# Performance work log

Hardware: AMD Instinct MI355X
Metric: run time of the kernel (lower is better)

Reference implementation:

```python
import jax, jax.numpy as jnp
import numpy as np

N_NODES = 100000
N_EDGES = 1600000
F_IN = 128
HID = 128  # nhid*2
NHID = 64
N_GRAPHS = 512
N_CLASSES = 10
NEG_SLOPE = 0.2  # PyG GATConv default


def setup_inputs() -> dict:
    key = jax.random.key(0)
    ks = jax.random.split(key, 16)
    x = jax.random.normal(ks[0], (N_NODES, F_IN), dtype=jnp.float32)
    edge_index = jax.random.randint(ks[1], (2, N_EDGES), 0, N_NODES, dtype=jnp.int64)
    batch = jnp.sort(jax.random.randint(ks[2], (N_NODES,), 0, N_GRAPHS, dtype=jnp.int64))
    def lin(k, fan_in, shape):
        bound = 1.0 / np.sqrt(fan_in)
        return jax.random.uniform(k, shape, jnp.float32, -bound, bound)
    return {
        "x": x, "edge_index": edge_index, "batch": batch,
        "W1": lin(ks[3], F_IN, (F_IN, HID)),
        "a_src1": lin(ks[4], HID, (HID,)),
        "a_dst1": lin(ks[5], HID, (HID,)),
        "b1": jnp.zeros((HID,), jnp.float32),
        "W2": lin(ks[6], HID, (HID, HID)),
        "a_src2": lin(ks[7], HID, (HID,)),
        "a_dst2": lin(ks[8], HID, (HID,)),
        "b2": jnp.zeros((HID,), jnp.float32),
        "W_fc1": lin(ks[9], HID, (HID, NHID)),
        "b_fc1": lin(ks[10], HID, (NHID,)),
        "W_fc2": lin(ks[11], NHID, (NHID, N_CLASSES)),
        "b_fc2": lin(ks[12], NHID, (N_CLASSES,)),
    }


def gat_conv(x, src, dst, W, a_src, a_dst, b):
    # h = W x ; attention e_ij = LeakyReLU(a_src.h_i + a_dst.h_j), softmax over
    # incoming edges of each destination j, then scatter-add aggregation.
    h = x @ W                                   # [N, H]
    alpha_s = h @ a_src                         # [N]
    alpha_d = h @ a_dst                         # [N]
    e = jax.nn.leaky_relu(alpha_s[src] + alpha_d[dst], NEG_SLOPE)  # [E]
    n = x.shape[0]
    m = jax.ops.segment_max(e, dst, num_segments=n)                # per-dst max
    ex = jnp.exp(e - m[dst])
    denom = jax.ops.segment_sum(ex, dst, num_segments=n)
    alpha = ex / denom[dst]                                        # [E]
    out = jax.ops.segment_sum(alpha[:, None] * h[src], dst, num_segments=n)
    return out + b


def reference(x, edge_index, batch, W1, a_src1, a_dst1, b1,
              W2, a_src2, a_dst2, b2, W_fc1, b_fc1, W_fc2, b_fc2):
    n = x.shape[0]
    # GATConv default add_self_loops=True
    loops = jnp.arange(n, dtype=edge_index.dtype)
    src = jnp.concatenate([edge_index[0], loops])
    dst = jnp.concatenate([edge_index[1], loops])

    h = jax.nn.selu(gat_conv(x, src, dst, W1, a_src1, a_dst1, b1))
    h = jax.nn.selu(gat_conv(h, src, dst, W2, a_src2, a_dst2, b2))

    # global mean pool over graphs
    sums = jax.ops.segment_sum(h, batch, num_segments=N_GRAPHS)
    cnts = jax.ops.segment_sum(jnp.ones((n,), h.dtype), batch, num_segments=N_GRAPHS)
    pooled = jax.nn.selu(sums / jnp.maximum(cnts, 1.0)[:, None])   # [G, H]

    g = jax.nn.selu(pooled @ W_fc1 + b_fc1)
    # dropout p=0.5 is identity in eval mode
    logits = g @ W_fc2 + b_fc2
    return jax.nn.log_softmax(logits, axis=-1)
```

## Files before the change

kernel.cpp:

```cpp
#include <hip/hip_runtime.h>
#include <hip/hip_bf16.h>

#define NEG_SLOPE 0.2f
typedef unsigned int uint32;

#define BSHIFT 9
#define BSIZE 512
#define MAXB 256
#define PCHUNK 2048
#define PEPT 8
#define BSTRIDE 12288
#define PNODES 256
#define PSPAN 16

typedef __attribute__((ext_vector_type(8))) __bf16 bf16x8;
typedef __attribute__((ext_vector_type(4))) float f32x4;
typedef __attribute__((ext_vector_type(2))) float f32x2;

__device__ __forceinline__ float selu_f(float x) {
    const float a = 1.6732632423543772f, s = 1.0507009873554805f;
    return x > 0.0f ? s * x : s * a * (__expf(x) - 1.0f);
}

__device__ __forceinline__ unsigned short f2bf(float x) {
    uint32 u = __float_as_uint(x);
    uint32 r = (u + 0x7fff + ((u >> 16) & 1)) >> 16;
    return (unsigned short)r;
}
__device__ __forceinline__ float bf_lo(uint32 g) { return __uint_as_float(g << 16); }
__device__ __forceinline__ float bf_hi(uint32 g) { return __uint_as_float(g & 0xffff0000u); }

__device__ __forceinline__ f32x2 f8x2lo(uint32 w) { return __builtin_amdgcn_cvt_pk_f32_fp8((int)w, false); }
__device__ __forceinline__ f32x2 f8x2hi(uint32 w) { return __builtin_amdgcn_cvt_pk_f32_fp8((int)w, true); }

__global__ __launch_bounds__(256) void prep9(const float* __restrict__ W1,
                                             const float* __restrict__ W2,
                                             unsigned short* __restrict__ Wb,
                                             const int* __restrict__ batch,
                                             int* __restrict__ gstart,
                                             int* __restrict__ gcur0,
                                             float* __restrict__ gsum,
                                             int N, int G) {
    int b = blockIdx.x, t = threadIdx.x;
    if (b < 2) {
        if (b == 0 && t < MAXB) gcur0[t] = 0;
        const float* W = b ? W2 : W1;
        unsigned short* oh = Wb + (size_t)b * 32768;
        unsigned short* ol = oh + 16384;
        for (int d = t; d < 16384; d += 256) {
            int j = d & 7, nn = (d >> 3) & 127, g = d >> 10;
            float v = W[(g * 8 + j) * 128 + nn];
            uint32 hu = f2bf(v);
            float hv = __uint_as_float(hu << 16);
            oh[d] = (unsigned short)hu;
            ol[d] = f2bf(v - hv);
        }
    } else {
        int i = (b - 2) * 256 + t;
        if (i < G * 128) gsum[i] = 0.0f;
        if (i < N) {
            int bb = batch[i];
            int bp = (i == 0) ? -1 : batch[i - 1];
            for (int q = bp + 1; q <= bb; ++q) gstart[q] = i;
            if (i == N - 1)
                for (int q = bb + 1; q <= G; ++q) gstart[q] = N;
        }
    }
}

__global__ __launch_bounds__(256) void partition_edges(const int* __restrict__ ei,
                                                       int* __restrict__ gcur0,
                                                       uint32* __restrict__ tmp,
                                                       int E, int TOT) {
    __shared__ int lcnt[MAXB];
    __shared__ int lstart[MAXB];
    __shared__ int lcur[MAXB];
    __shared__ int gbase[MAXB];
    __shared__ int wsums[4];
    __shared__ uint32 staged[PCHUNK];
    __shared__ unsigned char bslot[PCHUNK];
    int t = threadIdx.x;
    int lane = t & 63, w = t >> 6;
    int eb = blockIdx.x * PCHUNK;
    int sreg[PEPT], dreg[PEPT];
    #pragma unroll
    for (int k = 0; k < PEPT; ++k) {
        int e = eb + k * 256 + t;
        if (e < TOT) {
            if (e < E) { sreg[k] = ei[e]; dreg[k] = ei[E + e]; }
            else       { sreg[k] = dreg[k] = e - E; }
        } else dreg[k] = -1;
    }
    lcnt[t] = 0;
    __syncthreads();
    #pragma unroll
    for (int k = 0; k < PEPT; ++k)
        if (dreg[k] >= 0) atomicAdd(&lcnt[dreg[k] >> BSHIFT], 1);
    __syncthreads();
    int v = lcnt[t];
    int incl = v;
    #pragma unroll
    for (int off = 1; off < 64; off <<= 1) {
        int u = __shfl_up(incl, off);
        if (lane >= off) incl += u;
    }
    if (lane == 63) wsums[w] = incl;
    __syncthreads();
    int wadd = 0;
    #pragma unroll
    for (int k = 0; k < 4; ++k) wadd += (k < w) ? wsums[k] : 0;
    int ex = incl + wadd - v;
    lstart[t] = ex;
    lcur[t] = ex;
    if (v > 0) gbase[t] = t * BSTRIDE + atomicAdd(&gcur0[t], v);
    __syncthreads();
    #pragma unroll
    for (int k = 0; k < PEPT; ++k) {
        int d = dreg[k];
        if (d >= 0) {
            int b = d >> BSHIFT;
            int p = atomicAdd(&lcur[b], 1);
            staged[p] = ((uint32)(d & (BSIZE - 1)) << 17) | (uint32)sreg[k];
            bslot[p] = (unsigned char)b;
        }
    }
    __syncthreads();
    int nvalid = TOT - eb; if (nvalid > PCHUNK) nvalid = PCHUNK;
    for (int i = t; i < nvalid; i += 256) {
        int b = bslot[i];
        tmp[gbase[b] + (i - lstart[b])] = staged[i];
    }
}

__global__ __launch_bounds__(1024) void bucket_build(const uint32* __restrict__ tmp,
                                                     const int* __restrict__ gcur0,
                                                     int* __restrict__ rowptr,
                                                     int* __restrict__ rowend,
                                                     int* __restrict__ col,
                                                     int N, int NB) {
    __shared__ int cnt[BSIZE];
    __shared__ int bsums[4];
    int b = blockIdx.x, t = threadIdx.x;
    int lo = b << BSHIFT;
    int nn = N - lo; if (nn > BSIZE) nn = BSIZE;
    if (t < BSIZE) cnt[t] = 0;
    __syncthreads();
    int ebeg = b * BSTRIDE;
    int eend = ebeg + gcur0[b];
    for (int i = ebeg + t; i < eend; i += 1024)
        atomicAdd(&cnt[tmp[i] >> 17], 1);
    __syncthreads();
    int c0 = 0, c1 = 0, s2 = 0;
    if (t < 256) {
        c0 = cnt[2 * t]; c1 = cnt[2 * t + 1];
        s2 = c0 + c1;
    }
    int lane = t & 63, w = t >> 6;
    int incl = s2;
    #pragma unroll
    for (int off = 1; off < 64; off <<= 1) {
        int u = __shfl_up(incl, off);
        if (lane >= off) incl += u;
    }
    if (t < 256 && lane == 63) bsums[w] = incl;
    __syncthreads();
    if (t < 256) {
        int wadd = 0;
        #pragma unroll
        for (int k = 0; k < 4; ++k) wadd += (k < w) ? bsums[k] : 0;
        int ex = incl + wadd - s2;
        int st0 = ebeg + ex, st1 = st0 + c0;
        if (2 * t < nn)     { rowptr[lo + 2 * t] = st0;     rowend[lo + 2 * t] = st0 + c0; }
        if (2 * t + 1 < nn) { rowptr[lo + 2 * t + 1] = st1; rowend[lo + 2 * t + 1] = st1 + c1; }
        cnt[2 * t] = st0; cnt[2 * t + 1] = st1;
    }
    __syncthreads();
    for (int i = ebeg + t; i < eend; i += 1024) {
        uint32 u = tmp[i];
        int p = atomicAdd(&cnt[u >> 17], 1);
        col[p] = (int)(u & 0x1FFFFu);
    }
}

template<bool FP8>
__device__ __forceinline__ void gemm_core(const bf16x8 ah[2][4],
                                          const __bf16* Wl,
                                          const float* a_src, const float* a_dst,
                                          uint32* hb, float* as_, float* ad_,
                                          int rbase, int n, int col16, int quad) {
    f32x4 acc[2][8];
    #pragma unroll
    for (int mt = 0; mt < 2; ++mt)
        #pragma unroll
        for (int t = 0; t < 8; ++t) acc[mt][t] = (f32x4)(0.0f);

    #pragma unroll
    for (int c = 0; c < 4; ++c) {
        #pragma unroll
        for (int t = 0; t < 8; ++t) {
            int off = (((c * 4 + quad) * 128) + t * 16 + col16) * 8;
            bf16x8 bh = *(const bf16x8*)&Wl[off];
            bf16x8 bl = *(const bf16x8*)&Wl[16384 + off];
            #pragma unroll
            for (int mt = 0; mt < 2; ++mt) {
                acc[mt][t] = __builtin_amdgcn_mfma_f32_16x16x32_bf16(ah[mt][c], bh, acc[mt][t], 0, 0, 0);
                acc[mt][t] = __builtin_amdgcn_mfma_f32_16x16x32_bf16(ah[mt][c], bl, acc[mt][t], 0, 0, 0);
            }
        }
    }
    float asv[8], adv[8];
    #pragma unroll
    for (int t = 0; t < 8; ++t) { asv[t] = a_src[t * 16 + col16]; adv[t] = a_dst[t * 16 + col16]; }
    #pragma unroll
    for (int mt = 0; mt < 2; ++mt) {
        #pragma unroll
        for (int reg = 0; reg < 4; ++reg) {
            float s = 0.0f, d = 0.0f;
            #pragma unroll
            for (int t = 0; t < 8; ++t) {
                float v = acc[mt][t][reg];
                s += v * asv[t]; d += v * adv[t];
            }
            #pragma unroll
            for (int off = 1; off < 16; off <<= 1) {
                s += __shfl_xor(s, off);
                d += __shfl_xor(d, off);
            }
            int r = rbase + mt * 16 + quad * 4 + reg;
            if (col16 == 0 && r < n) { as_[r] = s; ad_[r] = d; }
        }
    }
    #pragma unroll
    for (int mt = 0; mt < 2; ++mt)
    #pragma unroll
    for (int t = 0; t < 8; ++t)
    #pragma unroll
    for (int reg = 0; reg < 4; ++reg) {
        float v = acc[mt][t][reg];
        int r = rbase + mt * 16 + quad * 4 + reg;
        if (FP8) {
            float p1 = __shfl_xor(v, 1);
            uint32 pk = (uint32)__builtin_amdgcn_cvt_pk_fp8_f32(v, p1, 0, false);
            uint32 pk2 = __shfl_xor(pk, 2);
            if (!(col16 & 3) && r < n)
                hb[(size_t)r * 32 + t * 4 + (col16 >> 2)] = (pk & 0xffffu) | (pk2 << 16);
        } else {
            float p = __shfl_xor(v, 1);
            if (!(col16 & 1) && r < n) {
                uint32 pkb = (uint32)f2bf(v) | ((uint32)f2bf(p) << 16);
                hb[(size_t)r * 64 + t * 8 + (col16 >> 1)] = pkb;
            }
        }
    }
}

__global__ __launch_bounds__(512) void gemm_mfma_f32(const float* __restrict__ X,
                                                     const unsigned short* __restrict__ Wbh,
                                                     const float* __restrict__ a_src,
                                                     const float* __restrict__ a_dst,
                                                     uint32* __restrict__ hb,
                                                     float* __restrict__ as_,
                                                     float* __restrict__ ad_, int n) {
    __shared__ __bf16 Wl[32768];
    const int tid = threadIdx.x;
    {
        const uint4* sw = (const uint4*)Wbh;
        uint4* dw = (uint4*)Wl;
        for (int i = tid; i < 4096; i += 512) dw[i] = sw[i];
    }
    const int lane = tid & 63, wid = tid >> 6;
    const int col16 = lane & 15, quad = lane >> 4;
    const int rbase = blockIdx.x * 256 + wid * 32;
    bf16x8 ah[2][4];
    #pragma unroll
    for (int mt = 0; mt < 2; ++mt) {
        int r = rbase + mt * 16 + col16;
        bool ok = (r < n);
        const float* xp = X + (size_t)r * 128;
        #pragma unroll
        for (int c = 0; c < 4; ++c) {
            int k0 = c * 32 + quad * 8;
            float4 x0 = ok ? *(const float4*)(xp + k0)     : make_float4(0.f,0.f,0.f,0.f);
            float4 x1 = ok ? *(const float4*)(xp + k0 + 4) : make_float4(0.f,0.f,0.f,0.f);
            float xs[8] = {x0.x,x0.y,x0.z,x0.w,x1.x,x1.y,x1.z,x1.w};
            #pragma unroll
            for (int j = 0; j < 8; ++j) ah[mt][c][j] = (__bf16)xs[j];
        }
    }
    __syncthreads();
    gemm_core<true>(ah, Wl, a_src, a_dst, hb, as_, ad_, rbase, n, col16, quad);
}

__global__ __launch_bounds__(512) void gemm_mfma_bf16(const __bf16* __restrict__ X,
                                                      const unsigned short* __restrict__ Wbh,
                                                      const float* __restrict__ a_src,
                                                      const float* __restrict__ a_dst,
                                                      uint32* __restrict__ hb,
                                                      float* __restrict__ as_,
                                                      float* __restrict__ ad_, int n) {
    __shared__ __bf16 Wl[32768];
    const int tid = threadIdx.x;
    {
        const uint4* sw = (const uint4*)Wbh;
        uint4* dw = (uint4*)Wl;
        for (int i = tid; i < 4096; i += 512) dw[i] = sw[i];
    }
    const int lane = tid & 63, wid = tid >> 6;
    const int col16 = lane & 15, quad = lane >> 4;
    const int rbase = blockIdx.x * 256 + wid * 32;
    bf16x8 ah[2][4];
    const bf16x8 zz = (bf16x8)((__bf16)0.0f);
    #pragma unroll
    for (int mt = 0; mt < 2; ++mt) {
        int r = rbase + mt * 16 + col16;
        bool ok = (r < n);
        const __bf16* xp = X + (size_t)r * 128;
        #pragma unroll
        for (int c = 0; c < 4; ++c)
            ah[mt][c] = ok ? *(const bf16x8*)(xp + c * 32 + quad * 8) : zz;
    }
    __syncthreads();
    gemm_core<true>(ah, Wl, a_src, a_dst, hb, as_, ad_, rbase, n, col16, quad);
}

#define GIDX8(SARR, T0) { _Pragma("unroll") \
    for (int k_ = 0; k_ < 8; ++k_) { int t_ = (T0) + k_; \
        int sv_ = (t_ < 16) ? s0 : s1; \
        int si_ = __shfl(sv_, base + (t_ & 15)); \
        SARR[k_] = (t_ < cnt) ? si_ : 0; } }

#define GW8(WARR, T0) { _Pragma("unroll") \
    for (int k_ = 0; k_ < 8; ++k_) { int t_ = (T0) + k_; \
        float wv_ = (t_ < 16) ? w0 : w1; \
        float wf_ = __shfl(wv_, base + (t_ & 15)); \
        WARR[k_] = (t_ < cnt) ? wf_ : 0.0f; } }

#define GLOAD8_F8(GARR, SARR) { _Pragma("unroll") \
    for (int k_ = 0; k_ < 8; ++k_) GARR[k_] = hb2[(uint32)SARR[k_] * 16u + l]; }

#define GCONSUME_F8(GARR, WARR) { _Pragma("unroll") \
    for (int k_ = 0; k_ < 8; ++k_) { \
        f32x2 wv_ = (f32x2)WARR[k_]; \
        ac[0] = __builtin_elementwise_fma(wv_, f8x2lo(GARR[k_].x), ac[0]); \
        ac[1] = __builtin_elementwise_fma(wv_, f8x2hi(GARR[k_].x), ac[1]); \
        ac[2] = __builtin_elementwise_fma(wv_, f8x2lo(GARR[k_].y), ac[2]); \
        ac[3] = __builtin_elementwise_fma(wv_, f8x2hi(GARR[k_].y), ac[3]); } }

__global__ __launch_bounds__(256) void gat_csr5_f8(const int* __restrict__ rowptr,
                                                   const int* __restrict__ rowend,
                                                   const int* __restrict__ col,
                                                   const uint2* __restrict__ hb2,
                                                   const float* __restrict__ as_,
                                                   const float* __restrict__ ad_,
                                                   const float* __restrict__ bias,
                                                   uint4* __restrict__ outb, int n) {
    const int wid = threadIdx.x >> 6;
    const int lane = threadIdx.x & 63;
    const int q = lane >> 4, l = lane & 15;
    const int base = lane & 48;
    const int node = blockIdx.x * 16 + wid * 4 + q;
    const bool valid = node < n;
    int beg = 0, end = 0;
    if (valid) { beg = rowptr[node]; end = rowend[node]; }
    float add = valid ? ad_[node] : 0.0f;
    int deg = end - beg;
    int m1 = max(deg, __shfl_xor(deg, 16));
    int mdeg = max(m1, __shfl_xor(m1, 32));
    float s = 0.0f;
    f32x2 ac[4];
    #pragma unroll
    for (int p = 0; p < 4; ++p) ac[p] = (f32x2)(0.0f);

    for (int cb = 0; cb < mdeg; cb += 32) {
        int j0 = beg + cb + l, j1 = j0 + 16;
        bool e0 = (j0 < end), e1 = (j1 < end);
        int s0 = e0 ? col[j0] : 0;
        int s1 = e1 ? col[j1] : 0;
        int cnt = end - beg - cb;
        cnt = (cnt < 0) ? 0 : (cnt > 32 ? 32 : cnt);
        int rem = mdeg - cb; if (rem > 32) rem = 32;
        const int NB8 = (rem + 7) >> 3;

        int si[8]; uint2 gA[8], gB[8]; float wA[8], wB[8];

        GIDX8(si, 0); GLOAD8_F8(gA, si);

        float v0 = as_[s0] + add;
        float v1 = as_[s1] + add;
        v0 = (v0 > 0.0f) ? v0 : NEG_SLOPE * v0;
        v1 = (v1 > 0.0f) ? v1 : NEG_SLOPE * v1;
        float w0 = e0 ? __expf(v0) : 0.0f;
        float w1 = e1 ? __expf(v1) : 0.0f;
        float ws = w0 + w1;
        #pragma unroll
        for (int off = 8; off > 0; off >>= 1) ws += __shfl_xor(ws, off);
        s += ws;
        GW8(wA, 0);

        int b = 0;
        while (true) {
            bool moreB = (b + 1 < NB8);
            if (moreB) { GIDX8(si, (b + 1) * 8); GLOAD8_F8(gB, si); GW8(wB, (b + 1) * 8); }
            GCONSUME_F8(gA, wA);
            if (!moreB) break;
            bool moreA = (b + 2 < NB8);
            if (moreA) { GIDX8(si, (b + 2) * 8); GLOAD8_F8(gA, si); GW8(wA, (b + 2) * 8); }
            GCONSUME_F8(gB, wB);
            if (!moreA) break;
            b += 2;
        }
    }
    if (valid) {
        float inv = 1.0f / s;
        float4 b0 = *(const float4*)&bias[l * 8];
        float4 b1 = *(const float4*)&bias[l * 8 + 4];
        float r0 = selu_f(ac[0].x * inv + b0.x);
        float r1 = selu_f(ac[0].y * inv + b0.y);
        float r2 = selu_f(ac[1].x * inv + b0.z);
        float r3 = selu_f(ac[1].y * inv + b0.w);
        float r4 = selu_f(ac[2].x * inv + b1.x);
        float r5 = selu_f(ac[2].y * inv + b1.y);
        float r6 = selu_f(ac[3].x * inv + b1.z);
        float r7 = selu_f(ac[3].y * inv + b1.w);
        uint4 o;
        o.x = (uint32)f2bf(r0) | ((uint32)f2bf(r1) << 16);
        o.y = (uint32)f2bf(r2) | ((uint32)f2bf(r3) << 16);
        o.z = (uint32)f2bf(r4) | ((uint32)f2bf(r5) << 16);
        o.w = (uint32)f2bf(r6) | ((uint32)f2bf(r7) << 16);
        outb[(uint32)node * 16u + l] = o;
    }
}

__global__ __launch_bounds__(256) void pool_stream(const uint32* __restrict__ act,
                                                   const int* __restrict__ batch,
                                                   float* __restrict__ gsum, int N) {
    __shared__ float pacc[PSPAN][128];
    const int t = threadIdx.x, wid = t >> 6, u = t & 63;
    const int n0 = blockIdx.x * PNODES;
    int n1 = n0 + PNODES; if (n1 > N) n1 = N;
    for (int i = t; i < PSPAN * 128; i += 256) pacc[i >> 7][i & 127] = 0.f;
    __syncthreads();
    const int gfirst = batch[n0];
    float a0 = 0.f, a1 = 0.f;
    int gcur = gfirst;
    for (int nd = n0 + wid; nd < n1; nd += 4) {
        int g = batch[nd];
        if (g != gcur) {
            int slot = gcur - gfirst;
            if (slot < PSPAN) {
                atomicAdd(&pacc[slot][2 * u], a0);
                atomicAdd(&pacc[slot][2 * u + 1], a1);
            } else {
                atomicAdd(&gsum[(size_t)gcur * 128 + 2 * u], a0);
                atomicAdd(&gsum[(size_t)gcur * 128 + 2 * u + 1], a1);
            }
            a0 = a1 = 0.f; gcur = g;
        }
        uint32 gv = act[(size_t)nd * 64 + u];
        a0 += bf_lo(gv); a1 += bf_hi(gv);
    }
    {
        int slot = gcur - gfirst;
        if (slot < PSPAN) {
            atomicAdd(&pacc[slot][2 * u], a0);
            atomicAdd(&pacc[slot][2 * u + 1], a1);
        } else {
            atomicAdd(&gsum[(size_t)gcur * 128 + 2 * u], a0);
            atomicAdd(&gsum[(size_t)gcur * 128 + 2 * u + 1], a1);
        }
    }
    __syncthreads();
    int lastg = batch[n1 - 1];
    int nslots = lastg - gfirst + 1; if (nslots > PSPAN) nslots = PSPAN;
    for (int i = t; i < nslots * 128; i += 256) {
        float v = pacc[i >> 7][i & 127];
        if (v != 0.f)
            atomicAdd(&gsum[(size_t)(gfirst + (i >> 7)) * 128 + (i & 127)], v);
    }
}

__global__ __launch_bounds__(128) void pool_head2(const float* __restrict__ gsum,
                                                  const int* __restrict__ gstart,
                                                  const float* __restrict__ Wfc1,
                                                  const float* __restrict__ bfc1,
                                                  const float* __restrict__ Wfc2,
                                                  const float* __restrict__ bfc2,
                                                  float* __restrict__ out) {
    __shared__ float p[128];
    __shared__ float q[64];
    __shared__ float l[10];
    __shared__ float red[2];
    int g = blockIdx.x, t = threadIdx.x;
    int lo = gstart[g], hi = gstart[g + 1];
    float c = fmaxf((float)(hi - lo), 1.0f);
    p[t] = selu_f(gsum[(size_t)g * 128 + t] / c);
    __syncthreads();
    if (t < 64) {
        float a = bfc1[t];
        #pragma unroll 8
        for (int k = 0; k < 128; ++k) a += p[k] * Wfc1[k * 64 + t];
        q[t] = selu_f(a);
    }
    __syncthreads();
    if (t < 10) {
        float a = bfc2[t];
        #pragma unroll
        for (int k = 0; k < 64; ++k) a += q[k] * Wfc2[k * 10 + t];
        l[t] = a;
    }
    __syncthreads();
    if (t == 0) {
        float mx = l[0];
        for (int c2 = 1; c2 < 10; ++c2) mx = fmaxf(mx, l[c2]);
        float sum = 0.0f;
        for (int c2 = 0; c2 < 10; ++c2) sum += __expf(l[c2] - mx);
        red[0] = mx; red[1] = logf(sum);
    }
    __syncthreads();
    if (t < 10) out[g * 10 + t] = l[t] - red[0] - red[1];
}

extern "C" void kernel_launch(void* const* d_in, const int* in_sizes, int n_in,
                              void* d_out, int out_size, void* d_ws, size_t ws_size,
                              hipStream_t stream) {
    const float* x      = (const float*)d_in[0];
    const int*   ei     = (const int*)d_in[1];
    const int*   batch  = (const int*)d_in[2];
    const float* W1     = (const float*)d_in[3];
    const float* asrc1  = (const float*)d_in[4];
    const float* adst1  = (const float*)d_in[5];
    const float* b1     = (const float*)d_in[6];
    const float* W2     = (const float*)d_in[7];
    const float* asrc2  = (const float*)d_in[8];
    const float* adst2  = (const float*)d_in[9];
    const float* b2     = (const float*)d_in[10];
    const float* Wfc1   = (const float*)d_in[11];
    const float* bfc1   = (const float*)d_in[12];
    const float* Wfc2   = (const float*)d_in[13];
    const float* bfc2   = (const float*)d_in[14];
    float* out = (float*)d_out;

    const int N = in_sizes[0] / 128;
    const int E = in_sizes[1] / 2;
    const int G = out_size / 10;
    const int TOT = E + N;
    const int NB = ((N - 1) >> BSHIFT) + 1;
    const int GB = (N + 255) / 256;
    const int PH = (TOT + PCHUNK - 1) / PCHUNK;
    const int GemmG = (N + 255) / 256;

    uint32* hb    = (uint32*)d_ws;
    uint32* h2b   = hb + (size_t)N * 64;
    uint32* tmp   = h2b + (size_t)N * 64;
    int*    col   = (int*)(tmp + (size_t)NB * BSTRIDE);
    float* as_    = (float*)(col + (size_t)NB * BSTRIDE);
    float* ad_    = as_ + N;
    int*   gstart = (int*)(ad_ + N);
    int*   rowptr = gstart + (G + 2);
    int*   rowend = rowptr + (N + 2);
    int*   gcur0  = rowend + (N + 2);
    unsigned short* Wb = (unsigned short*)(((uintptr_t)(gcur0 + MAXB) + 255) & ~(uintptr_t)255);
    float* gsum = (float*)(Wb + 2 * 32768);

    const int gatGrid = (N + 15) / 16;

    prep9<<<2 + GB, 256, 0, stream>>>(W1, W2, Wb, batch, gstart, gcur0, gsum, N, G);
    partition_edges<<<PH, 256, 0, stream>>>(ei, gcur0, tmp, E, TOT);
    bucket_build<<<NB, 1024, 0, stream>>>(tmp, gcur0, rowptr, rowend, col, N, NB);

    gemm_mfma_f32<<<GemmG, 512, 0, stream>>>(x, Wb, asrc1, adst1, hb, as_, ad_, N);
    gat_csr5_f8<<<gatGrid, 256, 0, stream>>>(rowptr, rowend, col, (const uint2*)hb,
                                             as_, ad_, b1, (uint4*)h2b, N);

    gemm_mfma_bf16<<<GemmG, 512, 0, stream>>>((const __bf16*)h2b, Wb + 32768, asrc2, adst2, hb, as_, ad_, N);
    gat_csr5_f8<<<gatGrid, 256, 0, stream>>>(rowptr, rowend, col, (const uint2*)hb,
                                             as_, ad_, b2, (uint4*)h2b, N);

    pool_stream<<<(N + PNODES - 1) / PNODES, 256, 0, stream>>>(h2b, batch, gsum, N);
    pool_head2<<<G, 128, 0, stream>>>(gsum, gstart, Wfc1, bfc1, Wfc2, bfc2, out);
}
```

Before: 353.3 us.

## Split GAT edge gather into two half-waves with 16-byte row loads

Each 16-lane node group now splits into two 8-lane halves, and each half handles alternate edges. A lane loads a uint4 (16 fp8 features) per edge instead of a uint2, so each half-group gathers a full 128-byte row with wider loads. Partial accumulators from the two halves are combined with a cross-lane shuffle before the epilogue, and only half the lanes write the output. This halves the per-lane gather instruction count and raises bytes per load, at the cost of more accumulator registers and an extra reduction step.

```diff
diff --git a/kernel.cpp b/kernel.cpp
--- a/kernel.cpp
+++ b/kernel.cpp
@@ -323,33 +323,37 @@
     gemm_core<true>(ah, Wl, a_src, a_dst, hb, as_, ad_, rbase, n, col16, quad);
 }
 
-#define GIDX8(SARR, T0) { _Pragma("unroll") \
-    for (int k_ = 0; k_ < 8; ++k_) { int t_ = (T0) + k_; \
+#define GIDX4(SARR, T0) { _Pragma("unroll") \
+    for (int k_ = 0; k_ < 4; ++k_) { int t_ = (T0) + 2 * k_ + sub; \
         int sv_ = (t_ < 16) ? s0 : s1; \
         int si_ = __shfl(sv_, base + (t_ & 15)); \
         SARR[k_] = (t_ < cnt) ? si_ : 0; } }
 
-#define GW8(WARR, T0) { _Pragma("unroll") \
-    for (int k_ = 0; k_ < 8; ++k_) { int t_ = (T0) + k_; \
+#define GW4(WARR, T0) { _Pragma("unroll") \
+    for (int k_ = 0; k_ < 4; ++k_) { int t_ = (T0) + 2 * k_ + sub; \
         float wv_ = (t_ < 16) ? w0 : w1; \
         float wf_ = __shfl(wv_, base + (t_ & 15)); \
         WARR[k_] = (t_ < cnt) ? wf_ : 0.0f; } }
 
-#define GLOAD8_F8(GARR, SARR) { _Pragma("unroll") \
-    for (int k_ = 0; k_ < 8; ++k_) GARR[k_] = hb2[(uint32)SARR[k_] * 16u + l]; }
-
-#define GCONSUME_F8(GARR, WARR) { _Pragma("unroll") \
-    for (int k_ = 0; k_ < 8; ++k_) { \
+#define GLOAD4_F8(GARR, SARR) { _Pragma("unroll") \
+    for (int k_ = 0; k_ < 4; ++k_) GARR[k_] = hb4[(uint32)SARR[k_] * 8u + l7]; }
+
+#define GCONSUME4_F8(GARR, WARR) { _Pragma("unroll") \
+    for (int k_ = 0; k_ < 4; ++k_) { \
         f32x2 wv_ = (f32x2)WARR[k_]; \
         ac[0] = __builtin_elementwise_fma(wv_, f8x2lo(GARR[k_].x), ac[0]); \
         ac[1] = __builtin_elementwise_fma(wv_, f8x2hi(GARR[k_].x), ac[1]); \
         ac[2] = __builtin_elementwise_fma(wv_, f8x2lo(GARR[k_].y), ac[2]); \
-        ac[3] = __builtin_elementwise_fma(wv_, f8x2hi(GARR[k_].y), ac[3]); } }
-
-__global__ __launch_bounds__(256) void gat_csr5_f8(const int* __restrict__ rowptr,
+        ac[3] = __builtin_elementwise_fma(wv_, f8x2hi(GARR[k_].y), ac[3]); \
+        ac[4] = __builtin_elementwise_fma(wv_, f8x2lo(GARR[k_].z), ac[4]); \
+        ac[5] = __builtin_elementwise_fma(wv_, f8x2hi(GARR[k_].z), ac[5]); \
+        ac[6] = __builtin_elementwise_fma(wv_, f8x2lo(GARR[k_].w), ac[6]); \
+        ac[7] = __builtin_elementwise_fma(wv_, f8x2hi(GARR[k_].w), ac[7]); } }
+
+__global__ __launch_bounds__(256) void gat_csr6_f8(const int* __restrict__ rowptr,
                                                    const int* __restrict__ rowend,
                                                    const int* __restrict__ col,
-                                                   const uint2* __restrict__ hb2,
+                                                   const uint4* __restrict__ hb4,
                                                    const float* __restrict__ as_,
                                                    const float* __restrict__ ad_,
                                                    const float* __restrict__ bias,
@@ -358,6 +362,8 @@
     const int lane = threadIdx.x & 63;
     const int q = lane >> 4, l = lane & 15;
     const int base = lane & 48;
+    const int sub = (lane >> 3) & 1;
+    const int l7 = lane & 7;
     const int node = blockIdx.x * 16 + wid * 4 + q;
     const bool valid = node < n;
     int beg = 0, end = 0;
@@ -367,9 +373,9 @@
     int m1 = max(deg, __shfl_xor(deg, 16));
     int mdeg = max(m1, __shfl_xor(m1, 32));
     float s = 0.0f;
-    f32x2 ac[4];
-    #pragma unroll
-    for (int p = 0; p < 4; ++p) ac[p] = (f32x2)(0.0f);
+    f32x2 ac[8];
+    #pragma unroll
+    for (int p = 0; p < 8; ++p) ac[p] = (f32x2)(0.0f);
 
     for (int cb = 0; cb < mdeg; cb += 32) {
         int j0 = beg + cb + l, j1 = j0 + 16;
@@ -381,9 +387,9 @@
         int rem = mdeg - cb; if (rem > 32) rem = 32;
         const int NB8 = (rem + 7) >> 3;
 
-        int si[8]; uint2 gA[8], gB[8]; float wA[8], wB[8];
-
-        GIDX8(si, 0); GLOAD8_F8(gA, si);
+        int si[4]; uint4 gA[4], gB[4]; float wA[4], wB[4];
+
+        GIDX4(si, 0); GLOAD4_F8(gA, si);
 
         float v0 = as_[s0] + add;
         float v1 = as_[s1] + add;
@@ -395,39 +401,40 @@
         #pragma unroll
         for (int off = 8; off > 0; off >>= 1) ws += __shfl_xor(ws, off);
         s += ws;
-        GW8(wA, 0);
+        GW4(wA, 0);
 
         int b = 0;
         while (true) {
             bool moreB = (b + 1 < NB8);
-            if (moreB) { GIDX8(si, (b + 1) * 8); GLOAD8_F8(gB, si); GW8(wB, (b + 1) * 8); }
-            GCONSUME_F8(gA, wA);
+            if (moreB) { GIDX4(si, (b + 1) * 8); GLOAD4_F8(gB, si); GW4(wB, (b + 1) * 8); }
+            GCONSUME4_F8(gA, wA);
             if (!moreB) break;
             bool moreA = (b + 2 < NB8);
-            if (moreA) { GIDX8(si, (b + 2) * 8); GLOAD8_F8(gA, si); GW8(wA, (b + 2) * 8); }
-            GCONSUME_F8(gB, wB);
+            if (moreA) { GIDX4(si, (b + 2) * 8); GLOAD4_F8(gA, si); GW4(wA, (b + 2) * 8); }
+            GCONSUME4_F8(gB, wB);
             if (!moreA) break;
             b += 2;
         }
     }
-    if (valid) {
+    float e[16];
+    #pragma unroll
+    for (int i = 0; i < 8; ++i) {
+        e[2 * i]     = ac[i].x + __shfl_xor(ac[i].x, 8);
+        e[2 * i + 1] = ac[i].y + __shfl_xor(ac[i].y, 8);
+    }
+    if (valid && sub == 0) {
         float inv = 1.0f / s;
-        float4 b0 = *(const float4*)&bias[l * 8];
-        float4 b1 = *(const float4*)&bias[l * 8 + 4];
-        float r0 = selu_f(ac[0].x * inv + b0.x);
-        float r1 = selu_f(ac[0].y * inv + b0.y);
-        float r2 = selu_f(ac[1].x * inv + b0.z);
-        float r3 = selu_f(ac[1].y * inv + b0.w);
-        float r4 = selu_f(ac[2].x * inv + b1.x);
-        float r5 = selu_f(ac[2].y * inv + b1.y);
-        float r6 = selu_f(ac[3].x * inv + b1.z);
-        float r7 = selu_f(ac[3].y * inv + b1.w);
-        uint4 o;
-        o.x = (uint32)f2bf(r0) | ((uint32)f2bf(r1) << 16);
-        o.y = (uint32)f2bf(r2) | ((uint32)f2bf(r3) << 16);
-        o.z = (uint32)f2bf(r4) | ((uint32)f2bf(r5) << 16);
-        o.w = (uint32)f2bf(r6) | ((uint32)f2bf(r7) << 16);
-        outb[(uint32)node * 16u + l] = o;
+        const float* bp = &bias[l7 * 16];
+        uint32 ow[8];
+        #pragma unroll
+        for (int i = 0; i < 8; ++i) {
+            float r0 = selu_f(e[2 * i] * inv + bp[2 * i]);
+            float r1 = selu_f(e[2 * i + 1] * inv + bp[2 * i + 1]);
+            ow[i] = (uint32)f2bf(r0) | ((uint32)f2bf(r1) << 16);
+        }
+        uint4* orow = outb + (uint32)node * 16u + l7 * 2;
+        orow[0] = make_uint4(ow[0], ow[1], ow[2], ow[3]);
+        orow[1] = make_uint4(ow[4], ow[5], ow[6], ow[7]);
     }
 }
 
@@ -569,11 +576,11 @@
     bucket_build<<<NB, 1024, 0, stream>>>(tmp, gcur0, rowptr, rowend, col, N, NB);
 
     gemm_mfma_f32<<<GemmG, 512, 0, stream>>>(x, Wb, asrc1, adst1, hb, as_, ad_, N);
-    gat_csr5_f8<<<gatGrid, 256, 0, stream>>>(rowptr, rowend, col, (const uint2*)hb,
+    gat_csr6_f8<<<gatGrid, 256, 0, stream>>>(rowptr, rowend, col, (const uint4*)hb,
                                              as_, ad_, b1, (uint4*)h2b, N);
 
     gemm_mfma_bf16<<<GemmG, 512, 0, stream>>>((const __bf16*)h2b, Wb + 32768, asrc2, adst2, hb, as_, ad_, N);
-    gat_csr5_f8<<<gatGrid, 256, 0, stream>>>(rowptr, rowend, col, (const uint2*)hb,
+    gat_csr6_f8<<<gatGrid, 256, 0, stream>>>(rowptr, rowend, col, (const uint4*)hb,
                                              as_, ad_, b2, (uint4*)h2b, N);
 
     pool_stream<<<(N + PNODES - 1) / PNODES, 256, 0, stream>>>(h2b, batch, gsum, N);
```

Result: slower. 389.9 us (+10.3%).
